# Optimization experiments

Hardware: AMD Instinct MI355X
Metric: run time of the kernel (lower is better)

Reference implementation:

```python
import jax, jax.numpy as jnp
import numpy as np

NUM_HEADS = 16

def setup_inputs() -> dict:
    key = jax.random.key(0)
    k1, k2, k3 = jax.random.split(key, 3)
    B, N, D = 2, 2048, 1024
    x = jax.random.normal(k1, (B, N, D), dtype=jnp.float32)
    w_qkv = jax.random.normal(k2, (D, 3 * D), dtype=jnp.float32) * (D ** -0.5)
    w_out = jax.random.normal(k3, (D, D), dtype=jnp.float32) * (D ** -0.5)
    return {"x": x, "w_qkv": w_qkv, "w_out": w_out}

def reference(x, w_qkv, w_out):
    B, N, D = x.shape
    H = NUM_HEADS
    d = D // H
    scale = d ** -0.5
    qkv = x @ w_qkv  # [B, N, 3D]
    q, k, v = jnp.split(qkv, 3, axis=-1)
    # b n (h d) -> b h n d
    split_heads = lambda t: t.reshape(B, N, H, d).transpose(0, 2, 1, 3)
    q, k, v = split_heads(q), split_heads(k), split_heads(v)
    dots = jnp.einsum('bhid,bhjd->bhij', q, k) * scale
    # causal mask: -inf above the diagonal
    causal = jnp.tril(jnp.ones((N, N), dtype=bool))
    dots = jnp.where(causal, dots, jnp.float32(-jnp.inf))
    attn = jax.nn.softmax(dots, axis=-1)
    out = jnp.einsum('bhij,bhjd->bhid', attn, v)
    out = out.transpose(0, 2, 1, 3).reshape(B, N, D)  # b h n d -> b n (h d)
    return out @ w_out
```

## Files before the change

### kernel.cpp

```cpp
#include <hip/hip_runtime.h>


typedef __bf16 bf16x8 __attribute__((ext_vector_type(8)));
typedef float f32x4 __attribute__((ext_vector_type(4)));
typedef unsigned int uint4v __attribute__((ext_vector_type(4)));

#define MFMA16(a, b, c) __builtin_amdgcn_mfma_f32_16x16x32_bf16((a), (b), (c), 0, 0, 0)

#define LDS_FENCE()                                   \
  do {                                                \
    asm volatile("s_waitcnt lgkmcnt(0)" ::: "memory");\
    __builtin_amdgcn_sched_barrier(0);                \
  } while (0)
#define LDS_ORDER()                                   \
  do {                                                \
    asm volatile("" ::: "memory");                    \
    __builtin_amdgcn_sched_barrier(0);                \
  } while (0)

__device__ __forceinline__ unsigned short f2bf(float f) {
  __bf16 h = (__bf16)f;
  return *(unsigned short*)&h;
}

__device__ __forceinline__ bf16x8 ones_frag() {
  uint4v u = {0x3F803F80u, 0x3F803F80u, 0x3F803F80u, 0x3F803F80u};
  return __builtin_bit_cast(bf16x8, u);
}

__global__ __launch_bounds__(256) void prep_kernel(
    const float* __restrict__ x, const float* __restrict__ wqkv,
    const float* __restrict__ wout, unsigned short* __restrict__ xb,
    unsigned short* __restrict__ wqkvT, unsigned short* __restrict__ woutT) {
  __shared__ float tile[32][33];
  const int id = blockIdx.x, t = threadIdx.x;
  if (id < 4096) {
    const int i = id * 256 + t;
    float4 v = ((const float4*)x)[i];
    ushort4 o;
    o.x = f2bf(v.x); o.y = f2bf(v.y); o.z = f2bf(v.z); o.w = f2bf(v.w);
    ((ushort4*)xb)[i] = o;
    return;
  }
  const int tx = t & 31, ty = t >> 5;
  const float* in; unsigned short* out;
  int C, scale_rows, bx, by;
  if (id < 7168) {
    const int q = id - 4096;
    in = wqkv; out = wqkvT; C = 3072; scale_rows = 1024;
    bx = q % 96; by = q / 96;
  } else {
    const int q = id - 7168;
    in = wout; out = woutT; C = 1024; scale_rows = 0;
    bx = q & 31; by = q >> 5;
  }
#pragma unroll
  for (int i = ty; i < 32; i += 8)
    tile[i][tx] = in[(size_t)(by * 32 + i) * C + bx * 32 + tx];
  __syncthreads();
#pragma unroll
  for (int i = ty; i < 32; i += 8) {
    const int orow = bx * 32 + i;
    const float s = (orow < scale_rows) ? 0.18033688f : 1.0f;
    out[(size_t)orow * 1024 + by * 32 + tx] = f2bf(tile[tx][i] * s);
  }
}

template <int MODE>
__global__ __launch_bounds__(256) void gemm128_kernel(
    const unsigned short* __restrict__ A,
    const unsigned short* __restrict__ BT,
    void* __restrict__ Cp, unsigned short* __restrict__ vTp,
    int M, int Nc, int K, int NX) {
  const int id0 = blockIdx.x;
  const int swz = (id0 & 7) * ((int)gridDim.x >> 3) + (id0 >> 3);
  const int bx = swz % NX, by = swz / NX;

  __shared__ unsigned short lA[128 * 64];
  __shared__ unsigned short lB[128 * 64];
  const int t = threadIdx.x;
  const int l = t & 63, g = l >> 4, c = l & 15;
  const int w = t >> 6;
  const int wm = (w >> 1) * 64, wn = (w & 1) * 64;
  const int bm = by * 128, bn = bx * 128;
  const int c7s = (c & 7);

  f32x4 acc[4][4] = {};

  for (int kk = 0; kk < K; kk += 64) {
    __syncthreads();
#pragma unroll
    for (int rd = 0; rd < 4; ++rd) {
      const int idx = rd * 256 + t;
      const int row = idx >> 3, ch = idx & 7;
      const int sc = (ch ^ (row & 7)) * 8;
      __builtin_amdgcn_global_load_lds(
          (const __attribute__((address_space(1))) void*)(
              A + (size_t)(bm + row) * K + kk + sc),
          (__attribute__((address_space(3))) void*)(lA + (idx & ~63) * 8),
          16, 0, 0);
      __builtin_amdgcn_global_load_lds(
          (const __attribute__((address_space(1))) void*)(
              BT + (size_t)(bn + row) * K + kk + sc),
          (__attribute__((address_space(3))) void*)(lB + (idx & ~63) * 8),
          16, 0, 0);
    }
    __syncthreads();

#pragma unroll
    for (int hh = 0; hh < 2; ++hh) {
      bf16x8 af[4], bfr[4];
#pragma unroll
      for (int mi = 0; mi < 4; ++mi)
        af[mi] = *(const bf16x8*)(lA + (wm + mi * 16 + c) * 64 +
                                  (((hh * 4 + g) ^ c7s) * 8));
#pragma unroll
      for (int ni = 0; ni < 4; ++ni)
        bfr[ni] = *(const bf16x8*)(lB + (wn + ni * 16 + c) * 64 +
                                   (((hh * 4 + g) ^ c7s) * 8));
#pragma unroll
      for (int mi = 0; mi < 4; ++mi)
#pragma unroll
        for (int ni = 0; ni < 4; ++ni)
          acc[mi][ni] = MFMA16(af[mi], bfr[ni], acc[mi][ni]);
    }
  }

  if (MODE == 0) {
    float* Cf = (float*)Cp;
#pragma unroll
    for (int mi = 0; mi < 4; ++mi)
#pragma unroll
      for (int r = 0; r < 4; ++r) {
        const int gr = bm + wm + mi * 16 + g * 4 + r;
#pragma unroll
        for (int ni = 0; ni < 4; ++ni)
          Cf[(size_t)gr * Nc + bn + wn + ni * 16 + c] = acc[mi][ni][r];
      }
  } else if (MODE == 2 && bn >= 2048) {
    const int bq = bm >> 11;
    const int nbase = bm - bq * 2048 + wm;
#pragma unroll
    for (int mi = 0; mi < 4; ++mi)
#pragma unroll
      for (int ni = 0; ni < 4; ++ni) {
        const int dimg = bn - 2048 + wn + ni * 16 + c;
        ushort4 pk;
        pk.x = f2bf(acc[mi][ni][0]); pk.y = f2bf(acc[mi][ni][1]);
        pk.z = f2bf(acc[mi][ni][2]); pk.w = f2bf(acc[mi][ni][3]);
        *(ushort4*)(vTp + ((size_t)(bq * 1024 + dimg)) * 2048 + nbase +
                    mi * 16 + g * 4) = pk;
      }
  } else {
    unsigned short* Cc = (unsigned short*)Cp;
#pragma unroll
    for (int mi = 0; mi < 4; ++mi)
#pragma unroll
      for (int r = 0; r < 4; ++r) {
        const int gr = bm + wm + mi * 16 + g * 4 + r;
#pragma unroll
        for (int ni = 0; ni < 4; ++ni)
          Cc[(size_t)gr * Nc + bn + wn + ni * 16 + c] = f2bf(acc[mi][ni][r]);
      }
  }
}

__global__ __launch_bounds__(256) void attn_kernel(
    const unsigned short* __restrict__ qkv,
    const unsigned short* __restrict__ vT,
    unsigned short* __restrict__ aout) {
  const int t = threadIdx.x, w = t >> 6, l = t & 63, g = l >> 4, c = l & 15;
  const int g4 = g * 4, c7 = c & 7;

  const int id0 = blockIdx.x;
  const int xcd = id0 & 7, pos = id0 >> 3;
  const int bh = xcd * 4 + (pos & 3);
  const int tile = 31 - (pos >> 2);
  const int b = bh >> 4, h = bh & 15;

  __shared__ __align__(16) unsigned short lK[2][64][64];
  __shared__ __align__(16) unsigned short lV[2][64][64];
  __shared__ __align__(16) unsigned short pl[4][16][72];

  const unsigned short* Qbase = qkv + (size_t)b * 2048 * 3072 + h * 64;
  const unsigned short* Kb = Qbase + 1024;
  const unsigned short* Vb = vT + ((size_t)b * 1024 + h * 64) * 2048;
  const bf16x8 vones = ones_frag();

#define KFRAG(row, half) (*(const bf16x8*)(Kb + (size_t)(row) * 3072 + (half) * 32 + g * 8))
#define VFRAG(dt, kvoff) (*(const bf16x8*)(Vb + (size_t)((dt) * 16 + c) * 2048 + (kvoff) + g * 8))

#define STAGE(dK, dV, kb_)                                                    \
  do {                                                                        \
    _Pragma("unroll")                                                         \
    for (int q = 0; q < 2; ++q) {                                             \
      const int idx = q * 256 + t;                                            \
      const int row = idx >> 3, ch = idx & 7;                                 \
      const int sc = (ch ^ (row & 7)) * 8;                                    \
      __builtin_amdgcn_global_load_lds(                                       \
          (const __attribute__((address_space(1))) void*)(                    \
              Kb + (size_t)(kb_ + row) * 3072 + sc),                          \
          (__attribute__((address_space(3))) void*)(                          \
              &(dK)[0][0] + (idx & ~63) * 8), 16, 0, 0);                      \
      __builtin_amdgcn_global_load_lds(                                       \
          (const __attribute__((address_space(1))) void*)(                    \
              Vb + (size_t)row * 2048 + (kb_) + sc),                          \
          (__attribute__((address_space(3))) void*)(                          \
              &(dV)[0][0] + (idx & ~63) * 8), 16, 0, 0);                      \
    }                                                                         \
  } while (0)

  const int q0 = tile * 64 + w * 16;
  const int qc = q0 + c;

  const bf16x8 bq0 = *(const bf16x8*)(Qbase + (size_t)qc * 3072 + g * 8);
  const bf16x8 bq1 = *(const bf16x8*)(Qbase + (size_t)qc * 3072 + 32 + g * 8);

  f32x4 o[4] = {};
  f32x4 dsum = {};

  if (tile > 0) {
    STAGE(lK[0], lV[0], 0);
    int cur = 0;
#pragma unroll 1
    for (int jb = 0; jb < tile; ++jb) {
      __syncthreads();
      if (jb + 1 < tile) STAGE(lK[cur ^ 1], lV[cur ^ 1], (jb + 1) * 64);

      const unsigned short* lk = &lK[cur][0][0];
      const unsigned short* lv = &lV[cur][0][0];

      bf16x8 ka[8];
#pragma unroll
      for (int n = 0; n < 4; ++n) {
        ka[2 * n]     = *(const bf16x8*)(lk + (16 * n + c) * 64 + ((g ^ c7) * 8));
        ka[2 * n + 1] = *(const bf16x8*)(lk + (16 * n + c) * 64 + (((4 + g) ^ c7) * 8));
      }
      bf16x8 bv[2][4];
#pragma unroll
      for (int ks = 0; ks < 2; ++ks)
#pragma unroll
        for (int dt = 0; dt < 4; ++dt)
          bv[ks][dt] = *(const bf16x8*)(lv + (dt * 16 + c) * 64 + (((ks * 4 + g) ^ c7) * 8));

      f32x4 s[4] = {};
#pragma unroll
      for (int n = 0; n < 4; ++n) {
        s[n] = MFMA16(ka[2 * n], bq0, s[n]);
        s[n] = MFMA16(ka[2 * n + 1], bq1, s[n]);
      }

#pragma unroll
      for (int n = 0; n < 4; ++n)
#pragma unroll
        for (int r = 0; r < 4; ++r)
          s[n][r] = exp2f(s[n][r]);

      LDS_ORDER();
#pragma unroll
      for (int n = 0; n < 4; ++n) {
        ushort4 pw;
        pw.x = f2bf(s[n][0]); pw.y = f2bf(s[n][1]);
        pw.z = f2bf(s[n][2]); pw.w = f2bf(s[n][3]);
        *(ushort4*)&pl[w][c][n * 16 + g4] = pw;
      }
      LDS_FENCE();
      const bf16x8 pa0 = *(const bf16x8*)&pl[w][c][g * 8];
      const bf16x8 pa1 = *(const bf16x8*)&pl[w][c][32 + g * 8];

      dsum = MFMA16(pa0, vones, dsum);
      dsum = MFMA16(pa1, vones, dsum);
#pragma unroll
      for (int dt = 0; dt < 4; ++dt) {
        o[dt] = MFMA16(pa0, bv[0][dt], o[dt]);
        o[dt] = MFMA16(pa1, bv[1][dt], o[dt]);
      }
      cur ^= 1;
    }
  }

  const int ndiag = 1 + (w >> 1);
#pragma unroll 1
  for (int j = 0; j < ndiag; ++j) {
    const int kb = tile * 64 + j * 32;
    const bf16x8 k00 = KFRAG(kb + c, 0), k01 = KFRAG(kb + c, 1);
    const bf16x8 k10 = KFRAG(kb + 16 + c, 0), k11 = KFRAG(kb + 16 + c, 1);
    const bf16x8 bv0 = VFRAG(0, kb), bv1 = VFRAG(1, kb);
    const bf16x8 bv2 = VFRAG(2, kb), bv3 = VFRAG(3, kb);

    f32x4 s0 = {}, s1 = {};
    s0 = MFMA16(k00, bq0, s0);
    s0 = MFMA16(k01, bq1, s0);
    s1 = MFMA16(k10, bq0, s1);
    s1 = MFMA16(k11, bq1, s1);

    float p0[4], p1[4];
#pragma unroll
    for (int r = 0; r < 4; ++r) {
      p0[r] = (kb + g4 + r <= qc) ? exp2f(s0[r]) : 0.0f;
      p1[r] = (kb + 16 + g4 + r <= qc) ? exp2f(s1[r]) : 0.0f;
    }

    LDS_ORDER();
    ushort4 pw;
    pw.x = f2bf(p0[0]); pw.y = f2bf(p0[1]); pw.z = f2bf(p0[2]); pw.w = f2bf(p0[3]);
    *(ushort4*)&pl[w][c][g4] = pw;
    pw.x = f2bf(p1[0]); pw.y = f2bf(p1[1]); pw.z = f2bf(p1[2]); pw.w = f2bf(p1[3]);
    *(ushort4*)&pl[w][c][16 + g4] = pw;
    LDS_FENCE();
    const bf16x8 pa = *(const bf16x8*)&pl[w][c][g * 8];

    dsum = MFMA16(pa, vones, dsum);
    o[0] = MFMA16(pa, bv0, o[0]);
    o[1] = MFMA16(pa, bv1, o[1]);
    o[2] = MFMA16(pa, bv2, o[2]);
    o[3] = MFMA16(pa, bv3, o[3]);
  }

#pragma unroll
  for (int r = 0; r < 4; ++r) {
    const float invr = 1.0f / dsum[r];
    const size_t row = (size_t)(b * 2048 + q0 + g4 + r);
#pragma unroll
    for (int dt = 0; dt < 4; ++dt)
      aout[row * 1024 + h * 64 + dt * 16 + c] = f2bf(o[dt][r] * invr);
  }
#undef KFRAG
#undef VFRAG
#undef STAGE
}

extern "C" void kernel_launch(void* const* d_in, const int* in_sizes, int n_in,
                              void* d_out, int out_size, void* d_ws, size_t ws_size,
                              hipStream_t stream) {
  const float* x = (const float*)d_in[0];
  const float* wqkv = (const float*)d_in[1];
  const float* wout = (const float*)d_in[2];
  float* out = (float*)d_out;

  unsigned short* ws = (unsigned short*)d_ws;
  unsigned short* xb = ws;
  unsigned short* wqkvT = xb + (size_t)4096 * 1024;
  unsigned short* woutT = wqkvT + (size_t)3072 * 1024;
  unsigned short* qkv = woutT + (size_t)1024 * 1024;
  unsigned short* vT = qkv + (size_t)4096 * 3072;
  unsigned short* aout = vT + (size_t)2 * 1024 * 2048;

  prep_kernel<<<8192, 256, 0, stream>>>(x, wqkv, wout, xb, wqkvT, woutT);
  gemm128_kernel<2><<<768, 256, 0, stream>>>(xb, wqkvT, qkv, vT, 4096, 3072, 1024, 24);
  attn_kernel<<<1024, 256, 0, stream>>>(qkv, vT, aout);
  gemm128_kernel<0><<<256, 256, 0, stream>>>(aout, woutT, out, nullptr, 4096, 1024, 1024, 8);
}
```

Baseline: 108.4 us.

## Triple-buffer K/V staging with partial vmcnt waits and shrink P scratch

Adds a third LDS buffer for K and V so the staging loads run two iterations ahead of the compute. The full __syncthreads is replaced by an explicit s_waitcnt vmcnt(4) plus a raw barrier, so only the oldest stage must have landed before the block syncs. The per-wave P scratch is cut in half by writing and reading the two 32-wide halves of P one after the other. The cost is more LDS per block, which could lower occupancy, and a second LDS fence inside the loop.

Result: slower. 110.7 us (+2.1%).

```diff
diff --git a/kernel.cpp b/kernel.cpp
--- a/kernel.cpp
+++ b/kernel.cpp
@@ -178,9 +178,9 @@
   const int tile = 31 - (pos >> 2);
   const int b = bh >> 4, h = bh & 15;
 
-  __shared__ __align__(16) unsigned short lK[2][64][64];
-  __shared__ __align__(16) unsigned short lV[2][64][64];
-  __shared__ __align__(16) unsigned short pl[4][16][72];
+  __shared__ __align__(16) unsigned short lK[3][64][64];
+  __shared__ __align__(16) unsigned short lV[3][64][64];
+  __shared__ __align__(16) unsigned short pl[4][16][40];
 
   const unsigned short* Qbase = qkv + (size_t)b * 2048 * 3072 + h * 64;
   const unsigned short* Kb = Qbase + 1024;
@@ -190,7 +190,7 @@
 #define KFRAG(row, half) (*(const bf16x8*)(Kb + (size_t)(row) * 3072 + (half) * 32 + g * 8))
 #define VFRAG(dt, kvoff) (*(const bf16x8*)(Vb + (size_t)((dt) * 16 + c) * 2048 + (kvoff) + g * 8))
 
-#define STAGE(dK, dV, kb_)                                                    \
+#define STAGE(bufi, kb_)                                                      \
   do {                                                                        \
     _Pragma("unroll")                                                         \
     for (int q = 0; q < 2; ++q) {                                             \
@@ -199,14 +199,14 @@
       const int sc = (ch ^ (row & 7)) * 8;                                    \
       __builtin_amdgcn_global_load_lds(                                       \
           (const __attribute__((address_space(1))) void*)(                    \
-              Kb + (size_t)(kb_ + row) * 3072 + sc),                          \
+              Kb + (size_t)((kb_) + row) * 3072 + sc),                        \
           (__attribute__((address_space(3))) void*)(                          \
-              &(dK)[0][0] + (idx & ~63) * 8), 16, 0, 0);                      \
+              &lK[bufi][0][0] + (idx & ~63) * 8), 16, 0, 0);                  \
       __builtin_amdgcn_global_load_lds(                                       \
           (const __attribute__((address_space(1))) void*)(                    \
-              Vb + (size_t)row * 2048 + (kb_) + sc),                          \
+              Vb + (size_t)row * 2048 + (kb_) + sc),                         \
           (__attribute__((address_space(3))) void*)(                          \
-              &(dV)[0][0] + (idx & ~63) * 8), 16, 0, 0);                      \
+              &lV[bufi][0][0] + (idx & ~63) * 8), 16, 0, 0);                  \
     }                                                                         \
   } while (0)
 
@@ -220,12 +220,22 @@
   f32x4 dsum = {};
 
   if (tile > 0) {
-    STAGE(lK[0], lV[0], 0);
+    STAGE(0, 0);
+    if (tile > 1) STAGE(1, 64);
     int cur = 0;
 #pragma unroll 1
     for (int jb = 0; jb < tile; ++jb) {
-      __syncthreads();
-      if (jb + 1 < tile) STAGE(lK[cur ^ 1], lV[cur ^ 1], (jb + 1) * 64);
+      if (jb + 1 < tile) {
+        asm volatile("s_waitcnt vmcnt(4)" ::: "memory");
+      } else {
+        asm volatile("s_waitcnt vmcnt(0)" ::: "memory");
+      }
+      __builtin_amdgcn_s_barrier();
+      __builtin_amdgcn_sched_barrier(0);
+      if (jb + 2 < tile) {
+        const int nb = (cur + 2 >= 3) ? cur - 1 : cur + 2;
+        STAGE(nb, (jb + 2) * 64);
+      }
 
       const unsigned short* lk = &lK[cur][0][0];
       const unsigned short* lv = &lV[cur][0][0];
@@ -258,7 +268,7 @@
 
       LDS_ORDER();
 #pragma unroll
-      for (int n = 0; n < 4; ++n) {
+      for (int n = 0; n < 2; ++n) {
         ushort4 pw;
         pw.x = f2bf(s[n][0]); pw.y = f2bf(s[n][1]);
         pw.z = f2bf(s[n][2]); pw.w = f2bf(s[n][3]);
@@ -266,7 +276,16 @@
       }
       LDS_FENCE();
       const bf16x8 pa0 = *(const bf16x8*)&pl[w][c][g * 8];
-      const bf16x8 pa1 = *(const bf16x8*)&pl[w][c][32 + g * 8];
+      LDS_ORDER();
+#pragma unroll
+      for (int n = 2; n < 4; ++n) {
+        ushort4 pw;
+        pw.x = f2bf(s[n][0]); pw.y = f2bf(s[n][1]);
+        pw.z = f2bf(s[n][2]); pw.w = f2bf(s[n][3]);
+        *(ushort4*)&pl[w][c][(n - 2) * 16 + g4] = pw;
+      }
+      LDS_FENCE();
+      const bf16x8 pa1 = *(const bf16x8*)&pl[w][c][g * 8];
 
       dsum = MFMA16(pa0, vones, dsum);
       dsum = MFMA16(pa1, vones, dsum);
@@ -275,7 +294,7 @@
         o[dt] = MFMA16(pa0, bv[0][dt], o[dt]);
         o[dt] = MFMA16(pa1, bv[1][dt], o[dt]);
       }
-      cur ^= 1;
+      cur = (cur + 1 >= 3) ? 0 : cur + 1;
     }
   }
 
```
